# Kernel tuning notes

Measured on AMD Instinct MI355X. Metric: run time of the kernel, lower is better.

## Reference

```python
import jax, jax.numpy as jnp
import numpy as np

N_NODES = 100000
N_EDGES = 50000
NNZ = 800000
C = 256
EPS = 0.0  # fixed (train_eps=False)


def setup_inputs() -> dict:
    key = jax.random.key(0)
    k1, k2, k3, k4, k5 = jax.random.split(key, 5)
    x_0 = jax.random.normal(k1, (N_NODES, C), dtype=jnp.float32)
    node_idx = jax.random.randint(k2, (NNZ,), 0, N_NODES, dtype=jnp.int64 if jax.config.jax_enable_x64 else jnp.int32)
    edge_idx = jax.random.randint(k3, (NNZ,), 0, N_EDGES, dtype=jnp.int64 if jax.config.jax_enable_x64 else jnp.int32)
    W = jax.random.normal(k4, (C, C), dtype=jnp.float32) / np.sqrt(C)
    b = jax.random.normal(k5, (C,), dtype=jnp.float32) * 0.01
    return {"x_0": x_0, "node_idx": node_idx, "edge_idx": edge_idx, "W": W, "b": b}


def reference(x_0, node_idx, edge_idx, W, b):
    # vertex2edge: x_1 = B_1^T @ x_0  (each hyperedge sums its member nodes)
    x_1 = jax.ops.segment_sum(x_0[node_idx], edge_idx, num_segments=N_EDGES)  # (E, C)
    # edge2vertex: m_{1->0} = B_1 @ x_1  (each node sums its incident hyperedges)
    m_1_0 = jax.ops.segment_sum(x_1[edge_idx], node_idx, num_segments=N_NODES)  # (N, C)
    # GIN update: Theta @ ((1+eps) x_0 + m)
    x_0_out = ((1.0 + EPS) * x_0 + m_1_0) @ W.T + b
    # use_norm=False -> no row normalization
    return (x_0_out, x_1)
```

## Files before the change

kernel.cpp:

```cpp
#include <hip/hip_runtime.h>

#define N_NODES 100000
#define N_EDGES 50000
#define NNZ     800000
#define C       256

#define SHC_E 8
#define SHC_N 9
#define NBC_E ((N_EDGES + (1 << SHC_E) - 1) >> SHC_E)
#define NBC_N ((N_NODES + (1 << SHC_N) - 1) >> SHC_N)
#define CHUNK 4096
#define NCHUNK ((NNZ + CHUNK - 1) / CHUNK)

#define CONV_BLOCKS (N_NODES * C / 4 / 256)

typedef short  bf16x8 __attribute__((ext_vector_type(8)));
typedef float  f32x4  __attribute__((ext_vector_type(4)));

static __device__ __forceinline__ unsigned short f2bf(float f) {
    unsigned int u = __float_as_uint(f);
    u += 0x7FFF + ((u >> 16) & 1);
    return (unsigned short)(u >> 16);
}
static __device__ __forceinline__ float bf2f(unsigned short u) {
    return __uint_as_float(((unsigned int)u) << 16);
}


__global__ void convert_hist(const float* __restrict__ x0, unsigned short* __restrict__ x0b,
                             const int* __restrict__ node_idx, const int* __restrict__ edge_idx,
                             int* __restrict__ gcnt_e, int* __restrict__ gcnt_n) {
    int bid = blockIdx.x;
    if (bid < CONV_BLOCKS) {
        size_t i = (size_t)bid * 256 + threadIdx.x;
        float4 v = ((const float4*)x0)[i];
        ushort4 o;
        o.x = f2bf(v.x); o.y = f2bf(v.y); o.z = f2bf(v.z); o.w = f2bf(v.w);
        ((ushort4*)x0b)[i] = o;
    } else {
        __shared__ int he[NBC_E], hn[NBC_N];
        const int tid = threadIdx.x;
        for (int i = tid; i < NBC_E; i += 256) he[i] = 0;
        for (int i = tid; i < NBC_N; i += 256) hn[i] = 0;
        __syncthreads();
        const int start = (bid - CONV_BLOCKS) * CHUNK;
        const int end = (start + CHUNK < NNZ) ? start + CHUNK : NNZ;
        for (int k = start + tid; k < end; k += 256) {
            atomicAdd(&he[edge_idx[k] >> SHC_E], 1);
            atomicAdd(&hn[node_idx[k] >> SHC_N], 1);
        }
        __syncthreads();
        for (int i = tid; i < NBC_E; i += 256) if (he[i]) atomicAdd(&gcnt_e[i], he[i]);
        for (int i = tid; i < NBC_N; i += 256) if (hn[i]) atomicAdd(&gcnt_n[i], hn[i]);
    }
}


__global__ void prep_w(const float* __restrict__ W, unsigned short* __restrict__ Wb) {
    int idx = blockIdx.x * 256 + threadIdx.x;
    int h = idx >> 12, i = idx & 4095;
    int t = i >> 9, s = (i >> 6) & 7, l = i & 63;
    int m = l & 15, q = l >> 4;
    const float* src = W + (size_t)(h * 128 + 16 * t + m) * C + 32 * s + 8 * q;
    float4 f0 = *(const float4*)(src);
    float4 f1 = *(const float4*)(src + 4);
    unsigned short* d = Wb + (size_t)idx * 8;
    d[0] = f2bf(f0.x); d[1] = f2bf(f0.y); d[2] = f2bf(f0.z); d[3] = f2bf(f0.w);
    d[4] = f2bf(f1.x); d[5] = f2bf(f1.y); d[6] = f2bf(f1.z); d[7] = f2bf(f1.w);
}


__global__ void coarse_scan(const int* __restrict__ gcnt_e, const int* __restrict__ gcnt_n,
                            int* __restrict__ gbase_e, int* __restrict__ gbase_n,
                            int* __restrict__ gcur_e, int* __restrict__ gcur_n) {
    const int* gcnt = (blockIdx.x == 0) ? gcnt_e : gcnt_n;
    int* gbase = (blockIdx.x == 0) ? gbase_e : gbase_n;
    int* gcur  = (blockIdx.x == 0) ? gcur_e : gcur_n;
    const int nb = (blockIdx.x == 0) ? NBC_E : NBC_N;
    int tid = threadIdx.x, lane = tid & 63, wid = tid >> 6;
    int v = (tid < nb) ? gcnt[tid] : 0;
    int incl = v;
#pragma unroll
    for (int s = 1; s < 64; s <<= 1) { int u = __shfl_up(incl, s, 64); if (lane >= s) incl += u; }
    __shared__ int wsum[4];
    if (lane == 63) wsum[wid] = incl;
    __syncthreads();
    int add = 0;
    for (int i = 0; i < wid; i++) add += wsum[i];
    int excl = add + incl - v;
    if (tid <= nb) gbase[tid] = excl;
    if (tid < nb)  gcur[tid]  = excl;
}


__global__ __launch_bounds__(256) void bin_coarse(const int* __restrict__ node_idx,
                                                  const int* __restrict__ edge_idx,
                                                  int* __restrict__ gcur_e, int* __restrict__ gcur_n,
                                                  unsigned int* __restrict__ tmp_e,
                                                  unsigned int* __restrict__ tmp_n) {
    __shared__ int hist_e[NBC_E], hist_n[NBC_N];
    __shared__ int base_e[NBC_E], base_n[NBC_N];
    const int tid = threadIdx.x;
    const int start = blockIdx.x * CHUNK;
    const int end = (start + CHUNK < NNZ) ? start + CHUNK : NNZ;

    for (int i = tid; i < NBC_E; i += 256) hist_e[i] = 0;
    for (int i = tid; i < NBC_N; i += 256) hist_n[i] = 0;
    __syncthreads();

    for (int k = start + tid; k < end; k += 256) {
        atomicAdd(&hist_e[edge_idx[k] >> SHC_E], 1);
        atomicAdd(&hist_n[node_idx[k] >> SHC_N], 1);
    }
    __syncthreads();

    for (int i = tid; i < NBC_E; i += 256) {
        int c = hist_e[i];
        base_e[i] = c ? atomicAdd(&gcur_e[i], c) : 0;
        hist_e[i] = 0;
    }
    for (int i = tid; i < NBC_N; i += 256) {
        int c = hist_n[i];
        base_n[i] = c ? atomicAdd(&gcur_n[i], c) : 0;
        hist_n[i] = 0;
    }
    __syncthreads();

    for (int k = start + tid; k < end; k += 256) {
        int ni = node_idx[k], ei = edge_idx[k];
        int be = ei >> SHC_E;
        int pe = base_e[be] + atomicAdd(&hist_e[be], 1);
        tmp_e[pe] = ((unsigned int)ni << SHC_E) | (unsigned int)(ei & ((1 << SHC_E) - 1));
        int bn = ni >> SHC_N;
        int pn = base_n[bn] + atomicAdd(&hist_n[bn], 1);
        tmp_n[pn] = ((unsigned int)ei << SHC_N) | (unsigned int)(ni & ((1 << SHC_N) - 1));
    }
}


template <int SHC, int NTOT>
static __device__ __forceinline__ void scatter_fine_body(const unsigned int* __restrict__ tmp,
                                                         const int* __restrict__ gbase,
                                                         int* __restrict__ off,
                                                         int* __restrict__ perm,
                                                         int b, int* hist, int* cur, int* wsum) {
    constexpr int NK = 1 << SHC;
    const int tid = threadIdx.x, lane = tid & 63, wid = tid >> 6;
    const int start = gbase[b], end = gbase[b + 1];
    for (int t = tid; t < NK; t += 256) hist[t] = 0;
    __syncthreads();
    for (int k = start + tid; k < end; k += 256)
        atomicAdd(&hist[tmp[k] & (NK - 1)], 1);
    __syncthreads();
    int v0, v1 = 0, local;
    if constexpr (NK == 512) { v0 = hist[2 * tid]; v1 = hist[2 * tid + 1]; local = v0 + v1; }
    else                     { v0 = hist[tid]; local = v0; }
    int incl = local;
#pragma unroll
    for (int s = 1; s < 64; s <<= 1) { int u = __shfl_up(incl, s, 64); if (lane >= s) incl += u; }
    if (lane == 63) wsum[wid] = incl;
    __syncthreads();
    int add = 0;
    for (int i = 0; i < wid; i++) add += wsum[i];
    int base = start + add + incl - local;
    const int kbase = b << SHC;
    if constexpr (NK == 512) {
        int key0 = kbase + 2 * tid;
        if (key0 < NTOT)     off[key0] = base;
        if (key0 + 1 < NTOT) off[key0 + 1] = base + v0;
        cur[2 * tid]     = base;
        cur[2 * tid + 1] = base + v0;
    } else {
        int key0 = kbase + tid;
        if (key0 < NTOT) off[key0] = base;
        cur[tid] = base;
    }
    if (b == ((NTOT - 1) >> SHC) && tid == 0) off[NTOT] = end;
    __syncthreads();
    for (int k = start + tid; k < end; k += 256) {
        unsigned int u = tmp[k];
        int pos = atomicAdd(&cur[u & (NK - 1)], 1);
        perm[pos] = (int)(u >> SHC);
    }
}

__global__ __launch_bounds__(256) void scatter_fine(const unsigned int* __restrict__ tmp_e,
                                                    const unsigned int* __restrict__ tmp_n,
                                                    const int* __restrict__ gbase_e,
                                                    const int* __restrict__ gbase_n,
                                                    int* __restrict__ off_e, int* __restrict__ off_n,
                                                    int* __restrict__ perm_e, int* __restrict__ perm_n) {
    __shared__ int hist[1 << SHC_N], cur[1 << SHC_N], wsum[4];
    if (blockIdx.x < NBC_E)
        scatter_fine_body<SHC_E, N_EDGES>(tmp_e, gbase_e, off_e, perm_e, blockIdx.x, hist, cur, wsum);
    else
        scatter_fine_body<SHC_N, N_NODES>(tmp_n, gbase_n, off_n, perm_n, blockIdx.x - NBC_E, hist, cur, wsum);
}


__global__ void pull_edge(const unsigned short* __restrict__ x0b,
                          const int* __restrict__ off, const int* __restrict__ perm,
                          float* __restrict__ x1, unsigned short* __restrict__ x1b) {
    int e = blockIdx.x * 4 + (threadIdx.x >> 6);
    int lane = threadIdx.x & 63;
    int s0 = off[e], s1 = off[e + 1];
    float a0 = 0, a1 = 0, a2 = 0, a3 = 0;
    float b0 = 0, b1 = 0, b2 = 0, b3 = 0;
    float c0 = 0, c1 = 0, c2 = 0, c3 = 0;
    float d0 = 0, d1 = 0, d2 = 0, d3 = 0;
    int k = s0;
    for (; k + 4 <= s1; k += 4) {
        int r0 = perm[k], r1 = perm[k + 1], r2 = perm[k + 2], r3 = perm[k + 3];
        ushort4 u0 = *(const ushort4*)(x0b + (size_t)r0 * C + lane * 4);
        ushort4 u1 = *(const ushort4*)(x0b + (size_t)r1 * C + lane * 4);
        ushort4 u2 = *(const ushort4*)(x0b + (size_t)r2 * C + lane * 4);
        ushort4 u3 = *(const ushort4*)(x0b + (size_t)r3 * C + lane * 4);
        a0 += bf2f(u0.x); a1 += bf2f(u0.y); a2 += bf2f(u0.z); a3 += bf2f(u0.w);
        b0 += bf2f(u1.x); b1 += bf2f(u1.y); b2 += bf2f(u1.z); b3 += bf2f(u1.w);
        c0 += bf2f(u2.x); c1 += bf2f(u2.y); c2 += bf2f(u2.z); c3 += bf2f(u2.w);
        d0 += bf2f(u3.x); d1 += bf2f(u3.y); d2 += bf2f(u3.z); d3 += bf2f(u3.w);
    }
    for (; k < s1; k++) {
        int r0 = perm[k];
        ushort4 u0 = *(const ushort4*)(x0b + (size_t)r0 * C + lane * 4);
        a0 += bf2f(u0.x); a1 += bf2f(u0.y); a2 += bf2f(u0.z); a3 += bf2f(u0.w);
    }
    a0 += b0 + c0 + d0; a1 += b1 + c1 + d1; a2 += b2 + c2 + d2; a3 += b3 + c3 + d3;
    f32x4 v = {a0, a1, a2, a3};
    __builtin_nontemporal_store(v, (f32x4*)(x1 + (size_t)e * C + lane * 4));
    ushort4 o; o.x = f2bf(a0); o.y = f2bf(a1); o.z = f2bf(a2); o.w = f2bf(a3);
    *(ushort4*)(x1b + (size_t)e * C + lane * 4) = o;
}

__global__ void pull_node(const float* __restrict__ x0, const unsigned short* __restrict__ x1b,
                          const int* __restrict__ off, const int* __restrict__ perm,
                          unsigned short* __restrict__ xm) {
    int n = blockIdx.x * 4 + (threadIdx.x >> 6);
    int lane = threadIdx.x & 63;
    int s0 = off[n], s1 = off[n + 1];
    const float4 x = *(const float4*)(x0 + (size_t)n * C + lane * 4);
    float a0 = x.x, a1 = x.y, a2 = x.z, a3 = x.w;
    float b0 = 0, b1 = 0, b2 = 0, b3 = 0;
    float c0 = 0, c1 = 0, c2 = 0, c3 = 0;
    float d0 = 0, d1 = 0, d2 = 0, d3 = 0;
    int k = s0;
    for (; k + 4 <= s1; k += 4) {
        int r0 = perm[k], r1 = perm[k + 1], r2 = perm[k + 2], r3 = perm[k + 3];
        ushort4 u0 = *(const ushort4*)(x1b + (size_t)r0 * C + lane * 4);
        ushort4 u1 = *(const ushort4*)(x1b + (size_t)r1 * C + lane * 4);
        ushort4 u2 = *(const ushort4*)(x1b + (size_t)r2 * C + lane * 4);
        ushort4 u3 = *(const ushort4*)(x1b + (size_t)r3 * C + lane * 4);
        a0 += bf2f(u0.x); a1 += bf2f(u0.y); a2 += bf2f(u0.z); a3 += bf2f(u0.w);
        b0 += bf2f(u1.x); b1 += bf2f(u1.y); b2 += bf2f(u1.z); b3 += bf2f(u1.w);
        c0 += bf2f(u2.x); c1 += bf2f(u2.y); c2 += bf2f(u2.z); c3 += bf2f(u2.w);
        d0 += bf2f(u3.x); d1 += bf2f(u3.y); d2 += bf2f(u3.z); d3 += bf2f(u3.w);
    }
    for (; k < s1; k++) {
        int r0 = perm[k];
        ushort4 u0 = *(const ushort4*)(x1b + (size_t)r0 * C + lane * 4);
        a0 += bf2f(u0.x); a1 += bf2f(u0.y); a2 += bf2f(u0.z); a3 += bf2f(u0.w);
    }
    a0 += b0 + c0 + d0; a1 += b1 + c1 + d1; a2 += b2 + c2 + d2; a3 += b3 + c3 + d3;
    ushort4 o; o.x = f2bf(a0); o.y = f2bf(a1); o.z = f2bf(a2); o.w = f2bf(a3);
    *(ushort4*)(xm + (size_t)n * C + lane * 4) = o;
}


__global__ __launch_bounds__(512) void mfma_gemm2(const unsigned short* __restrict__ xm,
                                                  const unsigned short* __restrict__ Wb,
                                                  const float* __restrict__ bias,
                                                  float* __restrict__ out) {
    __shared__ unsigned short Bs[8 * 8 * 64 * 8];
    const int rt = blockIdx.x >> 1;
    const int colbase = (blockIdx.x & 1) * 128;
    const int tid = threadIdx.x;

    const unsigned short* wsrc = Wb + (size_t)(blockIdx.x & 1) * (4096 * 8);
#pragma unroll
    for (int it = 0; it < 8; it++) {
        int i = it * 512 + tid;
        *(bf16x8*)(Bs + (size_t)i * 8) = *(const bf16x8*)(wsrc + (size_t)i * 8);
    }

    const int w = tid >> 6, lane = tid & 63;
    const int m = lane & 15, q = lane >> 4;
    const int row = rt * 128 + w * 16 + m;
    const int arow = row < N_NODES ? row : N_NODES - 1;

    bf16x8 a[8];
    const unsigned short* ap = xm + (size_t)arow * C + q * 8;
#pragma unroll
    for (int s = 0; s < 8; s++) a[s] = *(const bf16x8*)(ap + 32 * s);

    __syncthreads();

    f32x4 acc[8];
#pragma unroll
    for (int t = 0; t < 8; t++) acc[t] = (f32x4){0.f, 0.f, 0.f, 0.f};

#pragma unroll
    for (int s = 0; s < 8; s++) {
#pragma unroll
        for (int t = 0; t < 8; t++) {
            bf16x8 b = *(const bf16x8*)(Bs + ((t * 8 + s) * 64 + lane) * 8);
            acc[t] = __builtin_amdgcn_mfma_f32_16x16x32_bf16(a[s], b, acc[t], 0, 0, 0);
        }
    }

    const int r0 = rt * 128 + w * 16 + q * 4;
#pragma unroll
    for (int t = 0; t < 8; t++) {
        float bv = bias[colbase + t * 16 + m];
#pragma unroll
        for (int r = 0; r < 4; r++) {
            int rr = r0 + r;
            if (rr < N_NODES)
                out[(size_t)rr * C + colbase + t * 16 + m] = acc[t][r] + bv;
        }
    }
}


__global__ void init_kernel(const float* __restrict__ x0, float* __restrict__ out) {
    long long i = (long long)blockIdx.x * blockDim.x + threadIdx.x;
    const long long n_node4 = (long long)N_NODES * C / 4;
    const long long n_tot4  = (long long)(N_NODES + N_EDGES) * C / 4;
    float4* o4 = (float4*)out;
    if (i < n_node4)      o4[i] = ((const float4*)x0)[i];
    else if (i < n_tot4)  o4[i] = make_float4(0.f, 0.f, 0.f, 0.f);
}

__global__ void scatter_add_kernel(const float* __restrict__ src,
                                   const int* __restrict__ src_idx,
                                   const int* __restrict__ dst_idx,
                                   float* __restrict__ dst) {
    int j    = blockIdx.x * (blockDim.x >> 6) + (threadIdx.x >> 6);
    int lane = threadIdx.x & 63;
    if (j >= NNZ) return;
    int s = src_idx[j];
    int d = dst_idx[j];
    const float4 v = *(const float4*)(src + (long long)s * C + lane * 4);
    float* dp = dst + (long long)d * C + lane * 4;
    atomicAdd(dp + 0, v.x); atomicAdd(dp + 1, v.y);
    atomicAdd(dp + 2, v.z); atomicAdd(dp + 3, v.w);
}

__global__ void gin_gemm_kernel(const float* __restrict__ W,
                                const float* __restrict__ b,
                                float* __restrict__ out) {
    int n = blockIdx.x;
    int t = threadIdx.x;
    __shared__ float xs[C];
    float* row = out + (long long)n * C;
    xs[t] = row[t];
    __syncthreads();
    float acc = b[t];
    const float* wrow = W + t * C;
#pragma unroll 8
    for (int k = 0; k < C; k += 4) {
        float4 xv = *(const float4*)(xs + k);
        float4 wv = *(const float4*)(wrow + k);
        acc = fmaf(xv.x, wv.x, acc); acc = fmaf(xv.y, wv.y, acc);
        acc = fmaf(xv.z, wv.z, acc); acc = fmaf(xv.w, wv.w, acc);
    }
    row[t] = acc;
}


extern "C" void kernel_launch(void* const* d_in, const int* in_sizes, int n_in,
                              void* d_out, int out_size, void* d_ws, size_t ws_size,
                              hipStream_t stream) {
    const float* x0       = (const float*)d_in[0];
    const int*   node_idx = (const int*)d_in[1];
    const int*   edge_idx = (const int*)d_in[2];
    const float* W        = (const float*)d_in[3];
    const float* b        = (const float*)d_in[4];
    float* out = (float*)d_out;
    float* x1  = out + (size_t)N_NODES * C;

    char* p = (char*)d_ws;
    size_t used = 0;
    auto alloc = [&](size_t bytes) {
        char* r = p + used;
        used += (bytes + 255) & ~(size_t)255;
        return r;
    };
    int* off_e   = (int*)alloc((N_EDGES + 1) * 4);
    int* off_n   = (int*)alloc((N_NODES + 1) * 4);
    int* gcnt_e  = (int*)alloc(NBC_E * 4);
    int* gcnt_n  = (int*)alloc(NBC_N * 4);
    int* gbase_e = (int*)alloc((NBC_E + 1) * 4);
    int* gbase_n = (int*)alloc((NBC_N + 1) * 4);
    int* gcur_e  = (int*)alloc(NBC_E * 4);
    int* gcur_n  = (int*)alloc(NBC_N * 4);
    int* perm_e  = (int*)alloc((size_t)NNZ * 4);
    int* perm_n  = (int*)alloc((size_t)NNZ * 4);
    unsigned short* Wb  = (unsigned short*)alloc((size_t)2 * 4096 * 8 * 2);
    unsigned short* x0b = (unsigned short*)alloc((size_t)N_NODES * C * 2);
    unsigned short* x1b = (unsigned short*)alloc((size_t)N_EDGES * C * 2);
    unsigned short* xm  = (unsigned short*)alloc((size_t)N_NODES * C * 2);

    if (ws_size < used) {
        long long tot4 = (long long)(N_NODES + N_EDGES) * C / 4;
        init_kernel<<<(int)((tot4 + 255) / 256), 256, 0, stream>>>(x0, out);
        int grid = NNZ / 4;
        scatter_add_kernel<<<grid, 256, 0, stream>>>(x0, node_idx, edge_idx, x1);
        scatter_add_kernel<<<grid, 256, 0, stream>>>(x1, edge_idx, node_idx, out);
        gin_gemm_kernel<<<N_NODES, 256, 0, stream>>>(W, b, out);
        return;
    }

    hipMemsetAsync(gcnt_e, 0, (size_t)((char*)gcnt_n - (char*)gcnt_e) + (size_t)NBC_N * 4, stream);

    convert_hist<<<CONV_BLOCKS + NCHUNK, 256, 0, stream>>>(x0, x0b, node_idx, edge_idx,
                                                           gcnt_e, gcnt_n);

    prep_w<<<32, 256, 0, stream>>>(W, Wb);

    coarse_scan<<<2, 256, 0, stream>>>(gcnt_e, gcnt_n, gbase_e, gbase_n, gcur_e, gcur_n);

    unsigned int* tmp_e = (unsigned int*)x1b;
    unsigned int* tmp_n = (unsigned int*)xm;
    bin_coarse<<<NCHUNK, 256, 0, stream>>>(node_idx, edge_idx, gcur_e, gcur_n, tmp_e, tmp_n);
    scatter_fine<<<NBC_E + NBC_N, 256, 0, stream>>>(tmp_e, tmp_n, gbase_e, gbase_n,
                                                    off_e, off_n, perm_e, perm_n);

    pull_edge<<<N_EDGES / 4, 256, 0, stream>>>(x0b, off_e, perm_e, x1, x1b);
    pull_node<<<N_NODES / 4, 256, 0, stream>>>(x0, x1b, off_n, perm_n, xm);

    const int row_tiles = (N_NODES + 127) / 128;
    mfma_gemm2<<<row_tiles * 2, 512, 0, stream>>>(xm, Wb, b, out);
}
```

Baseline: 452.6 us.

## Reuse chunk histograms, fold prep_w, widen pull loads, use bf16 self term

The per-chunk coarse histograms computed in convert_hist are stored to global memory so bin_coarse no longer recomputes them, and the W conversion is folded into the same launch to drop one kernel. Both pull kernels now use 16-byte bf16x8 loads with two half-waves each handling alternating rows, combined with a cross-half shuffle. pull_node reads the self term from bf16 x0b instead of fp32 x0, which halves that read but adds rounding error. The GEMM output uses nontemporal stores.

```diff
diff --git a/kernel.cpp b/kernel.cpp
--- a/kernel.cpp
+++ b/kernel.cpp
@@ -13,6 +13,7 @@
 #define NCHUNK ((NNZ + CHUNK - 1) / CHUNK)
 
 #define CONV_BLOCKS (N_NODES * C / 4 / 256)
+#define PREPW_BLOCKS 32
 
 typedef short  bf16x8 __attribute__((ext_vector_type(8)));
 typedef float  f32x4  __attribute__((ext_vector_type(4)));
@@ -29,7 +30,9 @@
 
 __global__ void convert_hist(const float* __restrict__ x0, unsigned short* __restrict__ x0b,
                              const int* __restrict__ node_idx, const int* __restrict__ edge_idx,
-                             int* __restrict__ gcnt_e, int* __restrict__ gcnt_n) {
+                             int* __restrict__ gcnt_e, int* __restrict__ gcnt_n,
+                             int* __restrict__ chunkhist_e, int* __restrict__ chunkhist_n,
+                             const float* __restrict__ W, unsigned short* __restrict__ Wb) {
     int bid = blockIdx.x;
     if (bid < CONV_BLOCKS) {
         size_t i = (size_t)bid * 256 + threadIdx.x;
@@ -37,36 +40,42 @@
         ushort4 o;
         o.x = f2bf(v.x); o.y = f2bf(v.y); o.z = f2bf(v.z); o.w = f2bf(v.w);
         ((ushort4*)x0b)[i] = o;
-    } else {
+    } else if (bid < CONV_BLOCKS + NCHUNK) {
         __shared__ int he[NBC_E], hn[NBC_N];
         const int tid = threadIdx.x;
+        const int chunk = bid - CONV_BLOCKS;
         for (int i = tid; i < NBC_E; i += 256) he[i] = 0;
         for (int i = tid; i < NBC_N; i += 256) hn[i] = 0;
         __syncthreads();
-        const int start = (bid - CONV_BLOCKS) * CHUNK;
+        const int start = chunk * CHUNK;
         const int end = (start + CHUNK < NNZ) ? start + CHUNK : NNZ;
         for (int k = start + tid; k < end; k += 256) {
             atomicAdd(&he[edge_idx[k] >> SHC_E], 1);
             atomicAdd(&hn[node_idx[k] >> SHC_N], 1);
         }
         __syncthreads();
-        for (int i = tid; i < NBC_E; i += 256) if (he[i]) atomicAdd(&gcnt_e[i], he[i]);
-        for (int i = tid; i < NBC_N; i += 256) if (hn[i]) atomicAdd(&gcnt_n[i], hn[i]);
-    }
-}
-
-
-__global__ void prep_w(const float* __restrict__ W, unsigned short* __restrict__ Wb) {
-    int idx = blockIdx.x * 256 + threadIdx.x;
-    int h = idx >> 12, i = idx & 4095;
-    int t = i >> 9, s = (i >> 6) & 7, l = i & 63;
-    int m = l & 15, q = l >> 4;
-    const float* src = W + (size_t)(h * 128 + 16 * t + m) * C + 32 * s + 8 * q;
-    float4 f0 = *(const float4*)(src);
-    float4 f1 = *(const float4*)(src + 4);
-    unsigned short* d = Wb + (size_t)idx * 8;
-    d[0] = f2bf(f0.x); d[1] = f2bf(f0.y); d[2] = f2bf(f0.z); d[3] = f2bf(f0.w);
-    d[4] = f2bf(f1.x); d[5] = f2bf(f1.y); d[6] = f2bf(f1.z); d[7] = f2bf(f1.w);
+        for (int i = tid; i < NBC_E; i += 256) {
+            int c = he[i];
+            chunkhist_e[chunk * NBC_E + i] = c;
+            if (c) atomicAdd(&gcnt_e[i], c);
+        }
+        for (int i = tid; i < NBC_N; i += 256) {
+            int c = hn[i];
+            chunkhist_n[chunk * NBC_N + i] = c;
+            if (c) atomicAdd(&gcnt_n[i], c);
+        }
+    } else {
+        int idx = (bid - CONV_BLOCKS - NCHUNK) * 256 + threadIdx.x;
+        int h = idx >> 12, i = idx & 4095;
+        int t = i >> 9, s = (i >> 6) & 7, l = i & 63;
+        int m = l & 15, q = l >> 4;
+        const float* src = W + (size_t)(h * 128 + 16 * t + m) * C + 32 * s + 8 * q;
+        float4 f0 = *(const float4*)(src);
+        float4 f1 = *(const float4*)(src + 4);
+        unsigned short* d = Wb + (size_t)idx * 8;
+        d[0] = f2bf(f0.x); d[1] = f2bf(f0.y); d[2] = f2bf(f0.z); d[3] = f2bf(f0.w);
+        d[4] = f2bf(f1.x); d[5] = f2bf(f1.y); d[6] = f2bf(f1.z); d[7] = f2bf(f1.w);
+    }
 }
 
 
@@ -96,31 +105,24 @@
 __global__ __launch_bounds__(256) void bin_coarse(const int* __restrict__ node_idx,
                                                   const int* __restrict__ edge_idx,
                                                   int* __restrict__ gcur_e, int* __restrict__ gcur_n,
+                                                  const int* __restrict__ chunkhist_e,
+                                                  const int* __restrict__ chunkhist_n,
                                                   unsigned int* __restrict__ tmp_e,
                                                   unsigned int* __restrict__ tmp_n) {
     __shared__ int hist_e[NBC_E], hist_n[NBC_N];
     __shared__ int base_e[NBC_E], base_n[NBC_N];
     const int tid = threadIdx.x;
-    const int start = blockIdx.x * CHUNK;
+    const int chunk = blockIdx.x;
+    const int start = chunk * CHUNK;
     const int end = (start + CHUNK < NNZ) ? start + CHUNK : NNZ;
 
-    for (int i = tid; i < NBC_E; i += 256) hist_e[i] = 0;
-    for (int i = tid; i < NBC_N; i += 256) hist_n[i] = 0;
-    __syncthreads();
-
-    for (int k = start + tid; k < end; k += 256) {
-        atomicAdd(&hist_e[edge_idx[k] >> SHC_E], 1);
-        atomicAdd(&hist_n[node_idx[k] >> SHC_N], 1);
-    }
-    __syncthreads();
-
     for (int i = tid; i < NBC_E; i += 256) {
-        int c = hist_e[i];
+        int c = chunkhist_e[chunk * NBC_E + i];
         base_e[i] = c ? atomicAdd(&gcur_e[i], c) : 0;
         hist_e[i] = 0;
     }
     for (int i = tid; i < NBC_N; i += 256) {
-        int c = hist_n[i];
+        int c = chunkhist_n[chunk * NBC_N + i];
         base_n[i] = c ? atomicAdd(&gcur_n[i], c) : 0;
         hist_n[i] = 0;
     }
@@ -203,66 +205,101 @@
                           float* __restrict__ x1, unsigned short* __restrict__ x1b) {
     int e = blockIdx.x * 4 + (threadIdx.x >> 6);
     int lane = threadIdx.x & 63;
+    int half = lane >> 5;
+    int cl = lane & 31;
     int s0 = off[e], s1 = off[e + 1];
-    float a0 = 0, a1 = 0, a2 = 0, a3 = 0;
-    float b0 = 0, b1 = 0, b2 = 0, b3 = 0;
-    float c0 = 0, c1 = 0, c2 = 0, c3 = 0;
-    float d0 = 0, d1 = 0, d2 = 0, d3 = 0;
+    float a[8] = {0, 0, 0, 0, 0, 0, 0, 0};
+    float b[8] = {0, 0, 0, 0, 0, 0, 0, 0};
     int k = s0;
-    for (; k + 4 <= s1; k += 4) {
-        int r0 = perm[k], r1 = perm[k + 1], r2 = perm[k + 2], r3 = perm[k + 3];
-        ushort4 u0 = *(const ushort4*)(x0b + (size_t)r0 * C + lane * 4);
-        ushort4 u1 = *(const ushort4*)(x0b + (size_t)r1 * C + lane * 4);
-        ushort4 u2 = *(const ushort4*)(x0b + (size_t)r2 * C + lane * 4);
-        ushort4 u3 = *(const ushort4*)(x0b + (size_t)r3 * C + lane * 4);
-        a0 += bf2f(u0.x); a1 += bf2f(u0.y); a2 += bf2f(u0.z); a3 += bf2f(u0.w);
-        b0 += bf2f(u1.x); b1 += bf2f(u1.y); b2 += bf2f(u1.z); b3 += bf2f(u1.w);
-        c0 += bf2f(u2.x); c1 += bf2f(u2.y); c2 += bf2f(u2.z); c3 += bf2f(u2.w);
-        d0 += bf2f(u3.x); d1 += bf2f(u3.y); d2 += bf2f(u3.z); d3 += bf2f(u3.w);
-    }
-    for (; k < s1; k++) {
-        int r0 = perm[k];
-        ushort4 u0 = *(const ushort4*)(x0b + (size_t)r0 * C + lane * 4);
-        a0 += bf2f(u0.x); a1 += bf2f(u0.y); a2 += bf2f(u0.z); a3 += bf2f(u0.w);
-    }
-    a0 += b0 + c0 + d0; a1 += b1 + c1 + d1; a2 += b2 + c2 + d2; a3 += b3 + c3 + d3;
-    f32x4 v = {a0, a1, a2, a3};
-    __builtin_nontemporal_store(v, (f32x4*)(x1 + (size_t)e * C + lane * 4));
-    ushort4 o; o.x = f2bf(a0); o.y = f2bf(a1); o.z = f2bf(a2); o.w = f2bf(a3);
-    *(ushort4*)(x1b + (size_t)e * C + lane * 4) = o;
-}
-
-__global__ void pull_node(const float* __restrict__ x0, const unsigned short* __restrict__ x1b,
+    for (; k + 8 <= s1; k += 8) {
+        int r0 = perm[k + half],     r1 = perm[k + 2 + half];
+        int r2 = perm[k + 4 + half], r3 = perm[k + 6 + half];
+        bf16x8 u0 = *(const bf16x8*)(x0b + (size_t)r0 * C + cl * 8);
+        bf16x8 u1 = *(const bf16x8*)(x0b + (size_t)r1 * C + cl * 8);
+        bf16x8 u2 = *(const bf16x8*)(x0b + (size_t)r2 * C + cl * 8);
+        bf16x8 u3 = *(const bf16x8*)(x0b + (size_t)r3 * C + cl * 8);
+#pragma unroll
+        for (int j = 0; j < 8; j++) {
+            a[j] += bf2f((unsigned short)u0[j]); b[j] += bf2f((unsigned short)u1[j]);
+            a[j] += bf2f((unsigned short)u2[j]); b[j] += bf2f((unsigned short)u3[j]);
+        }
+    }
+    for (; k + 2 <= s1; k += 2) {
+        int r = perm[k + half];
+        bf16x8 u = *(const bf16x8*)(x0b + (size_t)r * C + cl * 8);
+#pragma unroll
+        for (int j = 0; j < 8; j++) a[j] += bf2f((unsigned short)u[j]);
+    }
+    if (k < s1 && half == 0) {
+        int r = perm[k];
+        bf16x8 u = *(const bf16x8*)(x0b + (size_t)r * C + cl * 8);
+#pragma unroll
+        for (int j = 0; j < 8; j++) a[j] += bf2f((unsigned short)u[j]);
+    }
+#pragma unroll
+    for (int j = 0; j < 8; j++) a[j] += b[j];
+#pragma unroll
+    for (int j = 0; j < 8; j++) a[j] += __shfl_down(a[j], 32);
+    if (half == 0) {
+        f32x4 vlo = {a[0], a[1], a[2], a[3]};
+        f32x4 vhi = {a[4], a[5], a[6], a[7]};
+        __builtin_nontemporal_store(vlo, (f32x4*)(x1 + (size_t)e * C + cl * 8));
+        __builtin_nontemporal_store(vhi, (f32x4*)(x1 + (size_t)e * C + cl * 8 + 4));
+        bf16x8 o;
+#pragma unroll
+        for (int j = 0; j < 8; j++) o[j] = (short)f2bf(a[j]);
+        *(bf16x8*)(x1b + (size_t)e * C + cl * 8) = o;
+    }
+}
+
+__global__ void pull_node(const unsigned short* __restrict__ x0b,
+                          const unsigned short* __restrict__ x1b,
                           const int* __restrict__ off, const int* __restrict__ perm,
                           unsigned short* __restrict__ xm) {
     int n = blockIdx.x * 4 + (threadIdx.x >> 6);
     int lane = threadIdx.x & 63;
+    int half = lane >> 5;
+    int cl = lane & 31;
     int s0 = off[n], s1 = off[n + 1];
-    const float4 x = *(const float4*)(x0 + (size_t)n * C + lane * 4);
-    float a0 = x.x, a1 = x.y, a2 = x.z, a3 = x.w;
-    float b0 = 0, b1 = 0, b2 = 0, b3 = 0;
-    float c0 = 0, c1 = 0, c2 = 0, c3 = 0;
-    float d0 = 0, d1 = 0, d2 = 0, d3 = 0;
+    float a[8] = {0, 0, 0, 0, 0, 0, 0, 0};
+    float b[8] = {0, 0, 0, 0, 0, 0, 0, 0};
     int k = s0;
-    for (; k + 4 <= s1; k += 4) {
-        int r0 = perm[k], r1 = perm[k + 1], r2 = perm[k + 2], r3 = perm[k + 3];
-        ushort4 u0 = *(const ushort4*)(x1b + (size_t)r0 * C + lane * 4);
-        ushort4 u1 = *(const ushort4*)(x1b + (size_t)r1 * C + lane * 4);
-        ushort4 u2 = *(const ushort4*)(x1b + (size_t)r2 * C + lane * 4);
-        ushort4 u3 = *(const ushort4*)(x1b + (size_t)r3 * C + lane * 4);
-        a0 += bf2f(u0.x); a1 += bf2f(u0.y); a2 += bf2f(u0.z); a3 += bf2f(u0.w);
-        b0 += bf2f(u1.x); b1 += bf2f(u1.y); b2 += bf2f(u1.z); b3 += bf2f(u1.w);
-        c0 += bf2f(u2.x); c1 += bf2f(u2.y); c2 += bf2f(u2.z); c3 += bf2f(u2.w);
-        d0 += bf2f(u3.x); d1 += bf2f(u3.y); d2 += bf2f(u3.z); d3 += bf2f(u3.w);
-    }
-    for (; k < s1; k++) {
-        int r0 = perm[k];
-        ushort4 u0 = *(const ushort4*)(x1b + (size_t)r0 * C + lane * 4);
-        a0 += bf2f(u0.x); a1 += bf2f(u0.y); a2 += bf2f(u0.z); a3 += bf2f(u0.w);
-    }
-    a0 += b0 + c0 + d0; a1 += b1 + c1 + d1; a2 += b2 + c2 + d2; a3 += b3 + c3 + d3;
-    ushort4 o; o.x = f2bf(a0); o.y = f2bf(a1); o.z = f2bf(a2); o.w = f2bf(a3);
-    *(ushort4*)(xm + (size_t)n * C + lane * 4) = o;
+    for (; k + 8 <= s1; k += 8) {
+        int r0 = perm[k + half],     r1 = perm[k + 2 + half];
+        int r2 = perm[k + 4 + half], r3 = perm[k + 6 + half];
+        bf16x8 u0 = *(const bf16x8*)(x1b + (size_t)r0 * C + cl * 8);
+        bf16x8 u1 = *(const bf16x8*)(x1b + (size_t)r1 * C + cl * 8);
+        bf16x8 u2 = *(const bf16x8*)(x1b + (size_t)r2 * C + cl * 8);
+        bf16x8 u3 = *(const bf16x8*)(x1b + (size_t)r3 * C + cl * 8);
+#pragma unroll
+        for (int j = 0; j < 8; j++) {
+            a[j] += bf2f((unsigned short)u0[j]); b[j] += bf2f((unsigned short)u1[j]);
+            a[j] += bf2f((unsigned short)u2[j]); b[j] += bf2f((unsigned short)u3[j]);
+        }
+    }
+    for (; k + 2 <= s1; k += 2) {
+        int r = perm[k + half];
+        bf16x8 u = *(const bf16x8*)(x1b + (size_t)r * C + cl * 8);
+#pragma unroll
+        for (int j = 0; j < 8; j++) a[j] += bf2f((unsigned short)u[j]);
+    }
+    if (k < s1 && half == 0) {
+        int r = perm[k];
+        bf16x8 u = *(const bf16x8*)(x1b + (size_t)r * C + cl * 8);
+#pragma unroll
+        for (int j = 0; j < 8; j++) a[j] += bf2f((unsigned short)u[j]);
+    }
+#pragma unroll
+    for (int j = 0; j < 8; j++) a[j] += b[j];
+#pragma unroll
+    for (int j = 0; j < 8; j++) a[j] += __shfl_down(a[j], 32);
+    if (half == 0) {
+        bf16x8 xr = *(const bf16x8*)(x0b + (size_t)n * C + cl * 8);
+        bf16x8 o;
+#pragma unroll
+        for (int j = 0; j < 8; j++) o[j] = (short)f2bf(a[j] + bf2f((unsigned short)xr[j]));
+        *(bf16x8*)(xm + (size_t)n * C + cl * 8) = o;
+    }
 }
 
 
@@ -315,7 +352,8 @@
         for (int r = 0; r < 4; r++) {
             int rr = r0 + r;
             if (rr < N_NODES)
-                out[(size_t)rr * C + colbase + t * 16 + m] = acc[t][r] + bv;
+                __builtin_nontemporal_store(acc[t][r] + bv,
+                                            out + (size_t)rr * C + colbase + t * 16 + m);
         }
     }
 }
@@ -393,6 +431,8 @@
     int* gbase_n = (int*)alloc((NBC_N + 1) * 4);
     int* gcur_e  = (int*)alloc(NBC_E * 4);
     int* gcur_n  = (int*)alloc(NBC_N * 4);
+    int* chunkhist_e = (int*)alloc((size_t)NCHUNK * NBC_E * 4);
+    int* chunkhist_n = (int*)alloc((size_t)NCHUNK * NBC_N * 4);
     int* perm_e  = (int*)alloc((size_t)NNZ * 4);
     int* perm_n  = (int*)alloc((size_t)NNZ * 4);
     unsigned short* Wb  = (unsigned short*)alloc((size_t)2 * 4096 * 8 * 2);
@@ -412,21 +452,20 @@
 
     hipMemsetAsync(gcnt_e, 0, (size_t)((char*)gcnt_n - (char*)gcnt_e) + (size_t)NBC_N * 4, stream);
 
-    convert_hist<<<CONV_BLOCKS + NCHUNK, 256, 0, stream>>>(x0, x0b, node_idx, edge_idx,
-                                                           gcnt_e, gcnt_n);
-
-    prep_w<<<32, 256, 0, stream>>>(W, Wb);
+    convert_hist<<<CONV_BLOCKS + NCHUNK + PREPW_BLOCKS, 256, 0, stream>>>(
+        x0, x0b, node_idx, edge_idx, gcnt_e, gcnt_n, chunkhist_e, chunkhist_n, W, Wb);
 
     coarse_scan<<<2, 256, 0, stream>>>(gcnt_e, gcnt_n, gbase_e, gbase_n, gcur_e, gcur_n);
 
     unsigned int* tmp_e = (unsigned int*)x1b;
     unsigned int* tmp_n = (unsigned int*)xm;
-    bin_coarse<<<NCHUNK, 256, 0, stream>>>(node_idx, edge_idx, gcur_e, gcur_n, tmp_e, tmp_n);
+    bin_coarse<<<NCHUNK, 256, 0, stream>>>(node_idx, edge_idx, gcur_e, gcur_n,
+                                           chunkhist_e, chunkhist_n, tmp_e, tmp_n);
     scatter_fine<<<NBC_E + NBC_N, 256, 0, stream>>>(tmp_e, tmp_n, gbase_e, gbase_n,
                                                     off_e, off_n, perm_e, perm_n);
 
     pull_edge<<<N_EDGES / 4, 256, 0, stream>>>(x0b, off_e, perm_e, x1, x1b);
-    pull_node<<<N_NODES / 4, 256, 0, stream>>>(x0, x1b, off_n, perm_n, xm);
+    pull_node<<<N_NODES / 4, 256, 0, stream>>>(x0b, x1b, off_n, perm_n, xm);
 
     const int row_tiles = (N_NODES + 127) / 128;
     mfma_gemm2<<<row_tiles * 2, 512, 0, stream>>>(xm, Wb, b, out);
```

New measurement: 432.2 us. -4.5%, faster.
